# Kernel optimization log

Hardware: AMD Instinct MI355X
Metric: run time of the kernel (lower is better)

## Reference

```python
import jax, jax.numpy as jnp
import numpy as np

B, N, C, H, L, WSZ = 4, 16384, 1024, 16, 256, 512
Dh = C // H
Nb = N // B
NW = Nb // WSZ
EPS = 1e-6
SCALE = Dh ** -0.5


def _ln(h, g=None, b=None):
    m = h.mean(-1, keepdims=True)
    v = h.var(-1, keepdims=True)
    h = (h - m) * jax.lax.rsqrt(v + EPS)
    if g is not None:
        h = h * g + b
    return h


def setup_inputs() -> dict:
    key = jax.random.key(0)
    ks = jax.random.split(key, 16)
    s = 0.02
    return {
        'x': jax.random.normal(ks[0], (N, C), jnp.float32),
        'context': jax.random.normal(ks[1], (B, L, C), jnp.float32),
        'mod': jax.random.normal(ks[2], (B, C), jnp.float32),
        'W_mod': jax.random.normal(ks[3], (C, 6 * C), jnp.float32) * s,
        'b_mod': jnp.zeros((6 * C,), jnp.float32),
        'gamma2': jnp.ones((C,), jnp.float32),
        'beta2': jnp.zeros((C,), jnp.float32),
        'W_qkv': jax.random.normal(ks[4], (C, 3 * C), jnp.float32) * s,
        'b_qkv': jnp.zeros((3 * C,), jnp.float32),
        'W_so': jax.random.normal(ks[5], (C, C), jnp.float32) * s,
        'b_so': jnp.zeros((C,), jnp.float32),
        'W_q': jax.random.normal(ks[6], (C, C), jnp.float32) * s,
        'b_q': jnp.zeros((C,), jnp.float32),
        'W_kv': jax.random.normal(ks[7], (C, 2 * C), jnp.float32) * s,
        'b_kv': jnp.zeros((2 * C,), jnp.float32),
        'W_co': jax.random.normal(ks[8], (C, C), jnp.float32) * s,
        'b_co': jnp.zeros((C,), jnp.float32),
        'W_m1': jax.random.normal(ks[9], (C, 4 * C), jnp.float32) * s,
        'b_m1': jnp.zeros((4 * C,), jnp.float32),
        'W_m2': jax.random.normal(ks[10], (4 * C, C), jnp.float32) * s,
        'b_m2': jnp.zeros((C,), jnp.float32),
    }


def reference(x, context, mod, W_mod, b_mod, gamma2, beta2, W_qkv, b_qkv,
              W_so, b_so, W_q, b_q, W_kv, b_kv, W_co, b_co,
              W_m1, b_m1, W_m2, b_m2):
    xb = x.reshape(B, Nb, C)

    # AdaLN modulation: SiLU -> Linear -> 6 chunks, broadcast per batch item
    m6 = jax.nn.silu(mod) @ W_mod + b_mod                   # [B, 6C]
    sh_msa, sc_msa, g_msa, sh_mlp, sc_mlp, g_mlp = jnp.split(m6, 6, axis=-1)

    # --- windowed sparse self-attention ---
    h = _ln(xb) * (1.0 + sc_msa[:, None]) + sh_msa[:, None]
    qkv = (h @ W_qkv + b_qkv).reshape(B, NW, WSZ, 3, H, Dh)
    q, k, v = qkv[:, :, :, 0], qkv[:, :, :, 1], qkv[:, :, :, 2]
    a = jax.nn.softmax(jnp.einsum('bwqhd,bwkhd->bwhqk', q, k) * SCALE, axis=-1)
    o = jnp.einsum('bwhqk,bwkhd->bwqhd', a, v).reshape(B, Nb, C)
    xb = xb + g_msa[:, None] * (o @ W_so + b_so)

    # --- full cross-attention to per-batch context ---
    h = _ln(xb, gamma2, beta2)
    q = (h @ W_q + b_q).reshape(B, Nb, H, Dh)
    kv = (context @ W_kv + b_kv).reshape(B, L, 2, H, Dh)
    k, v = kv[:, :, 0], kv[:, :, 1]
    a = jax.nn.softmax(jnp.einsum('bqhd,bkhd->bhqk', q, k) * SCALE, axis=-1)
    o = jnp.einsum('bhqk,bkhd->bqhd', a, v).reshape(B, Nb, C)
    xb = xb + (o @ W_co + b_co)

    # --- modulated sparse FFN ---
    h = _ln(xb) * (1.0 + sc_mlp[:, None]) + sh_mlp[:, None]
    h = jax.nn.gelu(h @ W_m1 + b_m1, approximate=True)
    xb = xb + g_mlp[:, None] * (h @ W_m2 + b_m2)

    return xb.reshape(N, C)
```

## Files before the change

kernel.cpp:

```cpp
#include <hip/hip_runtime.h>

typedef unsigned short u16;
typedef __attribute__((ext_vector_type(8))) short short8;
typedef __attribute__((ext_vector_type(4))) float f32x4;

#define SCALE_ 0.125f

struct __align__(8) U16x4 { u16 x, y, z, w; };

__device__ __forceinline__ u16 f2b(float f) {
  union { float f; unsigned u; } c; c.f = f;
  unsigned u = c.u;
  u += 0x7fffu + ((u >> 16) & 1u);
  return (u16)(u >> 16);
}

__device__ __forceinline__ void gload16(const void* g, void* l) {
  __builtin_amdgcn_global_load_lds((const __attribute__((address_space(1))) void*)g,
                                   (__attribute__((address_space(3))) void*)l,
                                   16, 0, 0);
}

__device__ __forceinline__ float gelu_t(float x) {
  float z = 1.5957691216057308f * (x + 0.044715f * x * x * x);
  return x / (1.0f + __expf(-z));
}

__global__ __launch_bounds__(256) void wcast(const float* __restrict__ W,
                                             u16* __restrict__ Wt, int K, int N) {
  __shared__ float t[32][33];
  const int nb = N >> 5;
  const int k0 = (blockIdx.x / nb) << 5;
  const int n0 = (blockIdx.x % nb) << 5;
  const int tx = threadIdx.x & 31;
  const int ty = threadIdx.x >> 5;
#pragma unroll
  for (int r = 0; r < 32; r += 8) t[ty + r][tx] = W[(size_t)(k0 + ty + r) * N + n0 + tx];
  __syncthreads();
#pragma unroll
  for (int r = 0; r < 32; r += 8) Wt[(size_t)(n0 + ty + r) * K + k0 + tx] = f2b(t[tx][ty + r]);
}

__global__ __launch_bounds__(256) void cast_bf(const float* __restrict__ in,
                                               u16* __restrict__ out) {
  const int i = blockIdx.x * 256 + threadIdx.x;
  const float4 v = ((const float4*)in)[i];
  U16x4 o; o.x = f2b(v.x); o.y = f2b(v.y); o.z = f2b(v.z); o.w = f2b(v.w);
  ((U16x4*)out)[i] = o;
}

__global__ __launch_bounds__(256) void mod_gemm(const float* __restrict__ mod,
                                                const float* __restrict__ Wm,
                                                const float* __restrict__ bm,
                                                float* __restrict__ m6) {
  __shared__ float s[4096];
  for (int i = threadIdx.x; i < 4096; i += 256) {
    float x = mod[i];
    s[i] = x / (1.0f + __expf(-x));
  }
  __syncthreads();
  const int j = blockIdx.x * 256 + threadIdx.x;
  float a0 = bm[j], a1 = a0, a2 = a0, a3 = a0;
#pragma unroll 8
  for (int c = 0; c < 1024; c++) {
    float w = Wm[(size_t)c * 6144 + j];
    a0 += s[c] * w;
    a1 += s[1024 + c] * w;
    a2 += s[2048 + c] * w;
    a3 += s[3072 + c] * w;
  }
  m6[j] = a0; m6[6144 + j] = a1; m6[12288 + j] = a2; m6[18432 + j] = a3;
}

__global__ __launch_bounds__(256) void ln_k(const float* __restrict__ x,
                                            u16* __restrict__ out,
                                            const float* __restrict__ g,
                                            const float* __restrict__ bb,
                                            int batch_stride, int add_one) {
  const int row = blockIdx.x;
  const int tid = threadIdx.x;
  const float4 v = ((const float4*)(x + (size_t)row * 1024))[tid];
  float s = v.x + v.y + v.z + v.w;
  float q = v.x * v.x + v.y * v.y + v.z * v.z + v.w * v.w;
#pragma unroll
  for (int m = 1; m < 64; m <<= 1) {
    s += __shfl_xor(s, m, 64);
    q += __shfl_xor(q, m, 64);
  }
  __shared__ float ps[4], pq[4];
  if ((tid & 63) == 0) { ps[tid >> 6] = s; pq[tid >> 6] = q; }
  __syncthreads();
  s = ps[0] + ps[1] + ps[2] + ps[3];
  q = pq[0] + pq[1] + pq[2] + pq[3];
  const float mean = s * (1.0f / 1024.0f);
  const float var = q * (1.0f / 1024.0f) - mean * mean;
  const float rstd = rsqrtf(var + 1e-6f);
  const int batch = row >> 12;
  const float4 gv = ((const float4*)(g + (size_t)batch * batch_stride))[tid];
  const float4 bv = ((const float4*)(bb + (size_t)batch * batch_stride))[tid];
  const float ao = add_one ? 1.0f : 0.0f;
  U16x4 o;
  o.x = f2b((v.x - mean) * rstd * (gv.x + ao) + bv.x);
  o.y = f2b((v.y - mean) * rstd * (gv.y + ao) + bv.y);
  o.z = f2b((v.z - mean) * rstd * (gv.z + ao) + bv.z);
  o.w = f2b((v.w - mean) * rstd * (gv.w + ao) + bv.w);
  ((U16x4*)(out + (size_t)row * 1024))[tid] = o;
}

template <int EPI>
__global__ __launch_bounds__(256) void gemm_bt(const u16* __restrict__ A,
                                               const u16* __restrict__ Bt,
                                               const float* __restrict__ bias,
                                               void* outp, const float* res,
                                               const float* gate, int M, int N,
                                               int K, int gate_stride) {
  __shared__ __align__(16) u16 As[4096];
  __shared__ __align__(16) u16 Bs[4096];
  const int nb = N >> 7;
  const int bm = (blockIdx.x / nb) << 7;
  const int bn = (blockIdx.x % nb) << 7;
  const int tid = threadIdx.x;
  const int lane = tid & 63;
  const int wv = tid >> 6;
  const int wr = (wv >> 1) << 6;
  const int wc = (wv & 1) << 6;
  const int lrow = lane & 15;
  const int lk = lane >> 4;
  const int srow = tid >> 2;
  const int scol = (tid & 3) << 3;
  const u16* gA = A + (size_t)(bm + srow) * K + scol;
  const u16* gB = Bt + (size_t)(bn + srow) * K + scol;
  const size_t rskip = (size_t)64 * K;
  u16* lA = As + wv * 512;
  u16* lB = Bs + wv * 512;
  f32x4 acc[4][4] = {};
  for (int k0 = 0; k0 < K; k0 += 32) {
    gload16(gA + k0, lA);
    gload16(gA + k0 + rskip, lA + 2048);
    gload16(gB + k0, lB);
    gload16(gB + k0 + rskip, lB + 2048);
    __syncthreads();
    short8 a[4], b[4];
#pragma unroll
    for (int m = 0; m < 4; m++)
      a[m] = *(const short8*)(As + (wr + m * 16 + lrow) * 32 + lk * 8);
#pragma unroll
    for (int n = 0; n < 4; n++)
      b[n] = *(const short8*)(Bs + (wc + n * 16 + lrow) * 32 + lk * 8);
#pragma unroll
    for (int m = 0; m < 4; m++)
#pragma unroll
      for (int n = 0; n < 4; n++)
        acc[m][n] = __builtin_amdgcn_mfma_f32_16x16x32_bf16(a[m], b[n], acc[m][n], 0, 0, 0);
    __syncthreads();
  }
#pragma unroll
  for (int m = 0; m < 4; m++) {
    const int row0 = bm + wr + m * 16 + lk * 4;
#pragma unroll
    for (int n = 0; n < 4; n++) {
      const int col = bn + wc + n * 16 + lrow;
      const float bval = bias[col];
#pragma unroll
      for (int j = 0; j < 4; j++) {
        float v = acc[m][n][j] + bval;
        size_t idx = (size_t)(row0 + j) * N + col;
        ((u16*)outp)[idx] = f2b(v);
      }
    }
  }
}

template <int EPI>
__global__ __launch_bounds__(512, 2) void gemm8p(const u16* __restrict__ A,
                                                 const u16* __restrict__ Bt,
                                                 const float* __restrict__ bias,
                                                 void* outp, const float* res,
                                                 const float* gate, int M, int N,
                                                 int K, int gate_stride) {
  extern __shared__ char smem[];
  const int nb = N >> 8;
  const int nwg = (M >> 8) * nb;
  const int cpx = nwg >> 3;
  const int wg = (blockIdx.x & 7) * cpx + (blockIdx.x >> 3);
  const int bm = (wg / nb) << 8;
  const int bn = (wg % nb) << 8;
  const int tid = threadIdx.x;
  const int lane = tid & 63;
  const int w = tid >> 6;
  const int wm = w >> 2;
  const int wn = w & 3;
  const int lrow = lane & 15;
  const int lk = lane >> 4;
  const int u = (lane & 7) ^ (lane >> 3);
  const int r_off = w * 16 + ((lane >> 3) << 1) + (u >> 2);
  const int c_off = (u & 3) << 3;
  const u16* gA = A + (size_t)(bm + r_off) * K + c_off;
  const u16* gB = Bt + (size_t)(bn + r_off) * K + c_off;
  const size_t l_skip = (size_t)128 * K;
  char* sA = smem;
  char* sB = smem + 65536;
  const int dsb = ((lrow >> 1) << 7) + (((((lrow & 1) << 2) + lk) ^ (lrow >> 1)) << 4);
  const int aQ = wm * 8192;
  const int bQ = wn * 4096;

  f32x4 acc[8][4] = {};
  short8 bq[4];
  short8 af[4];

#define SG_A(d, kh, tt)                                                         \
  { gload16(gA + (size_t)(tt) * 64 + (kh) * 32, sA + (d) * 32768 + (kh) * 16384 + w * 1024);            \
    gload16(gA + l_skip + (size_t)(tt) * 64 + (kh) * 32, sA + (d) * 32768 + (kh) * 16384 + (w + 8) * 1024); }
#define SG_B(d, kh, tt)                                                         \
  { gload16(gB + (size_t)(tt) * 64 + (kh) * 32, sB + (d) * 32768 + (kh) * 16384 + w * 1024);            \
    gload16(gB + l_skip + (size_t)(tt) * 64 + (kh) * 32, sB + (d) * 32768 + (kh) * 16384 + (w + 8) * 1024); }
#define RD_A(d, kh, mh)                                                         \
  _Pragma("unroll") for (int m = 0; m < 4; m++)                                 \
    af[m] = *(const short8*)(sA + (d) * 32768 + (kh) * 16384 + aQ + (mh) * 4096 + m * 1024 + dsb);
#define RD_B(d, kh)                                                             \
  _Pragma("unroll") for (int n = 0; n < 4; n++)                                 \
    bq[n] = *(const short8*)(sB + (d) * 32768 + (kh) * 16384 + bQ + n * 1024 + dsb);
#define MM(mh)                                                                  \
  _Pragma("unroll") for (int m = 0; m < 4; m++)                                 \
    _Pragma("unroll") for (int n = 0; n < 4; n++)                               \
      acc[(mh) * 4 + m][n] =                                                    \
          __builtin_amdgcn_mfma_f32_16x16x32_bf16(af[m], bq[n], acc[(mh) * 4 + m][n], 0, 0, 0);
#define SBAR0 __builtin_amdgcn_sched_barrier(0)
#define VM4   asm volatile("s_waitcnt vmcnt(4)" ::: "memory")

  SG_A(0, 0, 0); SG_B(0, 0, 0); SG_A(0, 1, 0); SG_B(0, 1, 0);
  SBAR0;
  VM4;
  __builtin_amdgcn_s_barrier();

  const int nt = K >> 6;
  for (int t = 0; t < nt; ++t) {
    const int d = t & 1;
    const int dn = d ^ 1;
    const int tn = (t + 1 < nt) ? t + 1 : t;
    {
      RD_A(d, 0, 0); RD_B(d, 0);
      SG_A(dn, 0, tn);
      __builtin_amdgcn_s_setprio(1);
      MM(0);
      __builtin_amdgcn_s_setprio(0);
      SBAR0;
    }
    {
      RD_A(d, 0, 1);
      SG_B(dn, 0, tn);
      SBAR0;
      VM4;
      __builtin_amdgcn_s_barrier();
      SBAR0;
      __builtin_amdgcn_s_setprio(1);
      MM(1);
      __builtin_amdgcn_s_setprio(0);
      SBAR0;
    }
    {
      RD_A(d, 1, 0); RD_B(d, 1);
      SG_A(dn, 1, tn);
      __builtin_amdgcn_s_setprio(1);
      MM(0);
      __builtin_amdgcn_s_setprio(0);
      SBAR0;
    }
    {
      RD_A(d, 1, 1);
      SG_B(dn, 1, tn);
      SBAR0;
      VM4;
      __builtin_amdgcn_s_barrier();
      SBAR0;
      __builtin_amdgcn_s_setprio(1);
      MM(1);
      __builtin_amdgcn_s_setprio(0);
      SBAR0;
    }
  }
  asm volatile("s_waitcnt vmcnt(0)" ::: "memory");
#undef SG_A
#undef SG_B
#undef RD_A
#undef RD_B
#undef MM
#undef SBAR0
#undef VM4

  const float* grow = nullptr;
  if (EPI == 2 && gate) grow = gate + (size_t)(bm >> 12) * gate_stride;
#pragma unroll
  for (int m = 0; m < 8; m++) {
    const int row0 = bm + wm * 128 + m * 16 + lk * 4;
#pragma unroll
    for (int n = 0; n < 4; n++) {
      const int col = bn + wn * 64 + n * 16 + lrow;
      const float bval = bias[col];
      float gval = 1.0f;
      if (EPI == 2 && grow) gval = grow[col];
#pragma unroll
      for (int j = 0; j < 4; j++) {
        float v = acc[m][n][j] + bval;
        size_t idx = (size_t)(row0 + j) * N + col;
        if (EPI == 0) {
          ((u16*)outp)[idx] = f2b(v);
        } else if (EPI == 1) {
          ((u16*)outp)[idx] = f2b(gelu_t(v));
        } else {
          ((float*)outp)[idx] = res[idx] + gval * v;
        }
      }
    }
  }
}

template <int MODE>
__global__ __launch_bounds__(512) void attn_k(const u16* __restrict__ QKV,
                                              const u16* __restrict__ Q2,
                                              const u16* __restrict__ KV2,
                                              u16* __restrict__ O) {
  __shared__ __align__(16) u16 Ks[4096];
  __shared__ __align__(16) u16 Vt[4096];
  __shared__ __align__(16) u16 Ps[16384];
  const int bid = blockIdx.x;
  const int tid = threadIdx.x;
  const int lane = tid & 63;
  const int wv = tid >> 6;
  const int lrow = lane & 15;
  const int lk = lane >> 4;
  const u16 *qp, *kp, *vp;
  int q_row0, q_stride, kv_row0, kv_stride, nkt, ocol;
  if (MODE == 0) {
    const int qt = bid & 1, h = (bid >> 1) & 15, w = (bid >> 5) & 7, b = bid >> 8;
    const int win = (b * 8 + w) * 512;
    q_row0 = win + qt * 256; q_stride = 3072;
    qp = QKV + h * 64;
    kp = QKV + 1024 + h * 64;
    vp = QKV + 2048 + h * 64;
    kv_row0 = win; kv_stride = 3072; nkt = 8;
    ocol = h * 64;
  } else {
    const int qt = bid & 15, h = (bid >> 4) & 15, b = bid >> 8;
    q_row0 = b * 4096 + qt * 256; q_stride = 1024;
    qp = Q2 + h * 64;
    kp = KV2 + h * 64;
    vp = KV2 + 1024 + h * 64;
    kv_row0 = b * 256; kv_stride = 2048; nkt = 4;
    ocol = h * 64;
  }
  const int qr = q_row0 + wv * 32;
  short8 qf[2][2];
#pragma unroll
  for (int m = 0; m < 2; m++)
#pragma unroll
    for (int kk = 0; kk < 2; kk++)
      qf[m][kk] = *(const short8*)(qp + (size_t)(qr + m * 16 + lrow) * q_stride + kk * 32 + lk * 8);
  f32x4 oa[2][4] = {};
  float lst[2][4];
#pragma unroll
  for (int m = 0; m < 2; m++)
#pragma unroll
    for (int j = 0; j < 4; j++) lst[m][j] = 0.0f;

  u16* Pw = Ps + wv * 2048;
  for (int kt = 0; kt < nkt; kt++) {
    const int kvr = kv_row0 + kt * 64;
    {
      const int r = tid >> 3, c = tid & 7;
      gload16(kp + (size_t)(kvr + r) * kv_stride + (((c) ^ (r & 7)) << 3),
              Ks + wv * 512);
    }
    {
      const int krow = tid >> 3, d0 = (tid & 7) << 3;
      short8 vvv = *(const short8*)(vp + (size_t)(kvr + krow) * kv_stride + d0);
#pragma unroll
      for (int i = 0; i < 8; i++) {
        const int ii = (i + (tid & 7)) & 7;
        const int dd = d0 + ii;
        Vt[dd * 64 + (((krow >> 3) ^ (dd & 7)) << 3) + (krow & 7)] = (u16)vvv[ii];
      }
    }
    __syncthreads();
    f32x4 s[2][4] = {};
    __builtin_amdgcn_s_setprio(1);
#pragma unroll
    for (int n = 0; n < 4; n++)
#pragma unroll
      for (int kk = 0; kk < 2; kk++) {
        short8 kb = *(const short8*)(Ks + (n * 16 + lrow) * 64 + (((kk * 4 + lk) ^ (lrow & 7)) << 3));
        s[0][n] = __builtin_amdgcn_mfma_f32_16x16x32_bf16(qf[0][kk], kb, s[0][n], 0, 0, 0);
        s[1][n] = __builtin_amdgcn_mfma_f32_16x16x32_bf16(qf[1][kk], kb, s[1][n], 0, 0, 0);
      }
    __builtin_amdgcn_s_setprio(0);
#pragma unroll
    for (int m = 0; m < 2; m++)
#pragma unroll
      for (int j = 0; j < 4; j++) {
        const float p0 = __expf(s[m][0][j] * SCALE_);
        const float p1 = __expf(s[m][1][j] * SCALE_);
        const float p2 = __expf(s[m][2][j] * SCALE_);
        const float p3 = __expf(s[m][3][j] * SCALE_);
        lst[m][j] += p0 + p1 + p2 + p3;
        const int prow = m * 16 + lk * 4 + j;
        const int base = prow * 64;
        const int r7 = prow & 7;
        const int kl = lrow >> 3, k7 = lrow & 7;
        Pw[base + (((0 + kl) ^ r7) << 3) + k7] = f2b(p0);
        Pw[base + (((2 + kl) ^ r7) << 3) + k7] = f2b(p1);
        Pw[base + (((4 + kl) ^ r7) << 3) + k7] = f2b(p2);
        Pw[base + (((6 + kl) ^ r7) << 3) + k7] = f2b(p3);
      }
#pragma unroll
    for (int kk = 0; kk < 2; kk++) {
      const int sw = ((kk * 4 + lk) ^ (lrow & 7)) << 3;
      short8 pa0 = *(const short8*)(Pw + lrow * 64 + sw);
      short8 pa1 = *(const short8*)(Pw + (16 + lrow) * 64 + sw);
      __builtin_amdgcn_s_setprio(1);
#pragma unroll
      for (int dn = 0; dn < 4; dn++) {
        short8 vb = *(const short8*)(Vt + (dn * 16 + lrow) * 64 + sw);
        oa[0][dn] = __builtin_amdgcn_mfma_f32_16x16x32_bf16(pa0, vb, oa[0][dn], 0, 0, 0);
        oa[1][dn] = __builtin_amdgcn_mfma_f32_16x16x32_bf16(pa1, vb, oa[1][dn], 0, 0, 0);
      }
      __builtin_amdgcn_s_setprio(0);
    }
    __syncthreads();
  }
#pragma unroll
  for (int m = 0; m < 2; m++)
#pragma unroll
    for (int j = 0; j < 4; j++) {
      float rs = lst[m][j];
      rs += __shfl_xor(rs, 1, 64);
      rs += __shfl_xor(rs, 2, 64);
      rs += __shfl_xor(rs, 4, 64);
      rs += __shfl_xor(rs, 8, 64);
      const float inv = 1.0f / rs;
      const int orow = qr + m * 16 + lk * 4 + j;
#pragma unroll
      for (int dn = 0; dn < 4; dn++)
        O[(size_t)orow * 1024 + ocol + dn * 16 + lrow] = f2b(oa[m][dn][j] * inv);
    }
}

extern "C" void kernel_launch(void* const* d_in, const int* in_sizes, int n_in,
                              void* d_out, int out_size, void* d_ws, size_t ws_size,
                              hipStream_t stream) {
  (void)in_sizes; (void)n_in; (void)out_size; (void)ws_size;
  const float* x      = (const float*)d_in[0];
  const float* ctx    = (const float*)d_in[1];
  const float* mod    = (const float*)d_in[2];
  const float* W_mod  = (const float*)d_in[3];
  const float* b_mod  = (const float*)d_in[4];
  const float* gamma2 = (const float*)d_in[5];
  const float* beta2  = (const float*)d_in[6];
  const float* W_qkv  = (const float*)d_in[7];
  const float* b_qkv  = (const float*)d_in[8];
  const float* W_so   = (const float*)d_in[9];
  const float* b_so   = (const float*)d_in[10];
  const float* W_q    = (const float*)d_in[11];
  const float* b_q    = (const float*)d_in[12];
  const float* W_kv   = (const float*)d_in[13];
  const float* b_kv   = (const float*)d_in[14];
  const float* W_co   = (const float*)d_in[15];
  const float* b_co   = (const float*)d_in[16];
  const float* W_m1   = (const float*)d_in[17];
  const float* b_m1   = (const float*)d_in[18];
  const float* W_m2   = (const float*)d_in[19];
  const float* b_m2   = (const float*)d_in[20];

  char* ws = (char*)d_ws;
  u16*   wt_qkv = (u16*)(ws + 0);
  u16*   wt_so  = (u16*)(ws + 6291456);
  u16*   wt_q   = (u16*)(ws + 8388608);
  u16*   wt_kv  = (u16*)(ws + 10485760);
  u16*   wt_co  = (u16*)(ws + 14680064);
  u16*   wt_m1  = (u16*)(ws + 16777216);
  u16*   wt_m2  = (u16*)(ws + 25165824);
  float* m6     = (float*)(ws + 33554432);
  u16*   ctxb   = (u16*)(ws + 33652736);
  u16*   kvb    = (u16*)(ws + 35749888);
  u16*   bufH   = (u16*)(ws + 39944192);
  u16*   bufO   = (u16*)(ws + 73498624);
  u16*   bufA   = (u16*)(ws + 107053056);
  float* xb1    = (float*)(ws + 107053056 + 50331648);
  float* outp   = (float*)d_out;

  hipFuncSetAttribute(reinterpret_cast<const void*>(&gemm8p<0>),
                      hipFuncAttributeMaxDynamicSharedMemorySize, 131072);
  hipFuncSetAttribute(reinterpret_cast<const void*>(&gemm8p<1>),
                      hipFuncAttributeMaxDynamicSharedMemorySize, 131072);
  hipFuncSetAttribute(reinterpret_cast<const void*>(&gemm8p<2>),
                      hipFuncAttributeMaxDynamicSharedMemorySize, 131072);

  wcast<<<3072, 256, 0, stream>>>(W_qkv, wt_qkv, 1024, 3072);
  wcast<<<1024, 256, 0, stream>>>(W_so,  wt_so,  1024, 1024);
  wcast<<<1024, 256, 0, stream>>>(W_q,   wt_q,   1024, 1024);
  wcast<<<2048, 256, 0, stream>>>(W_kv,  wt_kv,  1024, 2048);
  wcast<<<1024, 256, 0, stream>>>(W_co,  wt_co,  1024, 1024);
  wcast<<<4096, 256, 0, stream>>>(W_m1,  wt_m1,  1024, 4096);
  wcast<<<4096, 256, 0, stream>>>(W_m2,  wt_m2,  4096, 1024);
  cast_bf<<<1024, 256, 0, stream>>>(ctx, ctxb);

  mod_gemm<<<24, 256, 0, stream>>>(mod, W_mod, b_mod, m6);

  ln_k<<<16384, 256, 0, stream>>>(x, bufH, m6 + 1024, m6 + 0, 6144, 1);
  gemm8p<0><<<768, 512, 131072, stream>>>(bufH, wt_qkv, b_qkv, bufA, nullptr, nullptr, 16384, 3072, 1024, 0);
  attn_k<0><<<1024, 512, 0, stream>>>(bufA, nullptr, nullptr, bufO);
  gemm8p<2><<<256, 512, 131072, stream>>>(bufO, wt_so, b_so, xb1, x, m6 + 2048, 16384, 1024, 1024, 6144);

  ln_k<<<16384, 256, 0, stream>>>(xb1, bufH, gamma2, beta2, 0, 0);
  gemm8p<0><<<256, 512, 131072, stream>>>(bufH, wt_q, b_q, bufA, nullptr, nullptr, 16384, 1024, 1024, 0);
  gemm_bt<0><<<128, 256, 0, stream>>>(ctxb, wt_kv, b_kv, kvb, nullptr, nullptr, 1024, 2048, 1024, 0);
  attn_k<1><<<1024, 512, 0, stream>>>(nullptr, bufA, kvb, bufO);
  gemm8p<2><<<256, 512, 131072, stream>>>(bufO, wt_co, b_co, outp, xb1, nullptr, 16384, 1024, 1024, 0);

  ln_k<<<16384, 256, 0, stream>>>(outp, bufH, m6 + 4096, m6 + 3072, 6144, 1);
  gemm8p<1><<<1024, 512, 131072, stream>>>(bufH, wt_m1, b_m1, bufA, nullptr, nullptr, 16384, 4096, 1024, 0);
  gemm8p<2><<<256, 512, 131072, stream>>>(bufA, wt_m2, b_m2, outp, outp, m6 + 5120, 16384, 1024, 4096, 6144);
}
```

Before: 984.9 us.

## Double-buffer MFMA register fragments to overlap LDS reads with matrix math

Restructures the GEMM main loop so A and B fragments are held in two register sets (af0/af1, bq0/bq1). The LDS reads for the next sub-block, including the first fragments of the next K tile, are issued before the MFMAs on the current fragments. This is meant to hide LDS read latency behind MFMA work instead of stalling before each MFMA group, and it trims the barrier/priority bookkeeping. The cost is higher VGPR pressure, which could reduce occupancy or cause spills, plus a tighter dependence on barrier placement being correct for the reads that now cross tiles.

```diff
diff --git a/kernel.cpp b/kernel.cpp
--- a/kernel.cpp
+++ b/kernel.cpp
@@ -205,8 +205,7 @@
   const int bQ = wn * 4096;
 
   f32x4 acc[8][4] = {};
-  short8 bq[4];
-  short8 af[4];
+  short8 af0[4], af1[4], bq0[4], bq1[4];
 
 #define SG_A(d, kh, tt)                                                         \
   { gload16(gA + (size_t)(tt) * 64 + (kh) * 32, sA + (d) * 32768 + (kh) * 16384 + w * 1024);            \
@@ -214,17 +213,19 @@
 #define SG_B(d, kh, tt)                                                         \
   { gload16(gB + (size_t)(tt) * 64 + (kh) * 32, sB + (d) * 32768 + (kh) * 16384 + w * 1024);            \
     gload16(gB + l_skip + (size_t)(tt) * 64 + (kh) * 32, sB + (d) * 32768 + (kh) * 16384 + (w + 8) * 1024); }
-#define RD_A(d, kh, mh)                                                         \
+#define RD_AF(buf, d, kh, mh)                                                   \
   _Pragma("unroll") for (int m = 0; m < 4; m++)                                 \
-    af[m] = *(const short8*)(sA + (d) * 32768 + (kh) * 16384 + aQ + (mh) * 4096 + m * 1024 + dsb);
-#define RD_B(d, kh)                                                             \
+    buf[m] = *(const short8*)(sA + (d) * 32768 + (kh) * 16384 + aQ + (mh) * 4096 + m * 1024 + dsb);
+#define RD_BQ(buf, d, kh)                                                       \
   _Pragma("unroll") for (int n = 0; n < 4; n++)                                 \
-    bq[n] = *(const short8*)(sB + (d) * 32768 + (kh) * 16384 + bQ + n * 1024 + dsb);
-#define MM(mh)                                                                  \
+    buf[n] = *(const short8*)(sB + (d) * 32768 + (kh) * 16384 + bQ + n * 1024 + dsb);
+#define MM(mh, abuf, bbuf)                                                      \
+  __builtin_amdgcn_s_setprio(1);                                                \
   _Pragma("unroll") for (int m = 0; m < 4; m++)                                 \
     _Pragma("unroll") for (int n = 0; n < 4; n++)                               \
       acc[(mh) * 4 + m][n] =                                                    \
-          __builtin_amdgcn_mfma_f32_16x16x32_bf16(af[m], bq[n], acc[(mh) * 4 + m][n], 0, 0, 0);
+          __builtin_amdgcn_mfma_f32_16x16x32_bf16(abuf[m], bbuf[n], acc[(mh) * 4 + m][n], 0, 0, 0); \
+  __builtin_amdgcn_s_setprio(0);
 #define SBAR0 __builtin_amdgcn_sched_barrier(0)
 #define VM4   asm volatile("s_waitcnt vmcnt(4)" ::: "memory")
 
@@ -232,58 +233,40 @@
   SBAR0;
   VM4;
   __builtin_amdgcn_s_barrier();
+  SBAR0;
+  RD_AF(af0, 0, 0, 0); RD_BQ(bq0, 0, 0);
 
   const int nt = K >> 6;
   for (int t = 0; t < nt; ++t) {
     const int d = t & 1;
     const int dn = d ^ 1;
     const int tn = (t + 1 < nt) ? t + 1 : t;
-    {
-      RD_A(d, 0, 0); RD_B(d, 0);
-      SG_A(dn, 0, tn);
-      __builtin_amdgcn_s_setprio(1);
-      MM(0);
-      __builtin_amdgcn_s_setprio(0);
-      SBAR0;
-    }
-    {
-      RD_A(d, 0, 1);
-      SG_B(dn, 0, tn);
-      SBAR0;
-      VM4;
-      __builtin_amdgcn_s_barrier();
-      SBAR0;
-      __builtin_amdgcn_s_setprio(1);
-      MM(1);
-      __builtin_amdgcn_s_setprio(0);
-      SBAR0;
-    }
-    {
-      RD_A(d, 1, 0); RD_B(d, 1);
-      SG_A(dn, 1, tn);
-      __builtin_amdgcn_s_setprio(1);
-      MM(0);
-      __builtin_amdgcn_s_setprio(0);
-      SBAR0;
-    }
-    {
-      RD_A(d, 1, 1);
-      SG_B(dn, 1, tn);
-      SBAR0;
-      VM4;
-      __builtin_amdgcn_s_barrier();
-      SBAR0;
-      __builtin_amdgcn_s_setprio(1);
-      MM(1);
-      __builtin_amdgcn_s_setprio(0);
-      SBAR0;
-    }
+    RD_AF(af1, d, 0, 1);
+    SG_A(dn, 0, tn);
+    MM(0, af0, bq0);
+    SG_B(dn, 0, tn);
+    SBAR0;
+    VM4;
+    __builtin_amdgcn_s_barrier();
+    SBAR0;
+    RD_AF(af0, d, 1, 0); RD_BQ(bq1, d, 1);
+    MM(1, af1, bq0);
+    RD_AF(af1, d, 1, 1);
+    SG_A(dn, 1, tn);
+    MM(0, af0, bq1);
+    SG_B(dn, 1, tn);
+    SBAR0;
+    VM4;
+    __builtin_amdgcn_s_barrier();
+    SBAR0;
+    RD_AF(af0, dn, 0, 0); RD_BQ(bq0, dn, 0);
+    MM(1, af1, bq1);
   }
   asm volatile("s_waitcnt vmcnt(0)" ::: "memory");
 #undef SG_A
 #undef SG_B
-#undef RD_A
-#undef RD_B
+#undef RD_AF
+#undef RD_BQ
 #undef MM
 #undef SBAR0
 #undef VM4
```

Measured after the change: 1.004 ms. Within noise of the previous version (+1.9%).
